# Performance work log

Measured on AMD Instinct MI355X. Metric: run time of the kernel, lower is better.

Reference implementation:

```python
import jax, jax.numpy as jnp
import numpy as np

N = 100_000      # nodes
E = 1_600_000    # edges (before self-loops)
F_IN = 128       # num_features
H = 128          # nhid
G = 512          # graphs in batch
C = 10           # num_classes
EPS = 1e-5       # BatchNorm eps


def setup_inputs() -> dict:
    key = jax.random.key(0)
    ks = jax.random.split(key, 24)
    x = jax.random.normal(ks[0], (N, F_IN), jnp.float32)
    edge_index = jax.random.randint(ks[1], (2, E), 0, N, dtype=jnp.int64)
    batch = jnp.sort(jax.random.randint(ks[2], (N,), 0, G, dtype=jnp.int64))

    def lin(k, fi, fo):
        return jax.random.normal(k, (fi, fo), jnp.float32) / np.sqrt(fi).astype(np.float32)

    inp = dict(x=x, edge_index=edge_index, batch=batch)
    inp.update(
        W1=lin(ks[3], F_IN, H), b1=jnp.zeros((H,), jnp.float32),
        g1=jnp.ones((H,), jnp.float32), be1=jnp.zeros((H,), jnp.float32),
        W2=lin(ks[4], H, H), b2=jnp.zeros((H,), jnp.float32),
        g2=jnp.ones((H,), jnp.float32), be2=jnp.zeros((H,), jnp.float32),
        W3=lin(ks[5], H, H), b3=jnp.zeros((H,), jnp.float32),
        g3=jnp.ones((H,), jnp.float32), be3=jnp.zeros((H,), jnp.float32),
        gp=jnp.ones((H,), jnp.float32), bep=jnp.zeros((H,), jnp.float32),
        lw1=lin(ks[6], H, H), lb1=jnp.zeros((H,), jnp.float32),
        lw2=lin(ks[7], H, C), lb2=jnp.zeros((C,), jnp.float32),
    )
    return inp


def _batchnorm(h, g, b):
    # training-mode BatchNorm1d: batch stats, biased variance
    m = h.mean(axis=0)
    v = h.var(axis=0)
    return g * (h - m) * jax.lax.rsqrt(v + EPS) + b


def _gcn(h, W, b, src, dst, norm, n):
    # GCNConv: h @ W, then normalized gather-scatter aggregation
    h = h @ W
    msg = h[src] * norm[:, None]                     # [E+N, H] gather
    out = jax.ops.segment_sum(msg, dst, num_segments=n)
    return out + b


def reference(x, edge_index, batch, W1, b1, g1, be1, W2, b2, g2, be2,
              W3, b3, g3, be3, gp, bep, lw1, lb1, lw2, lb2):
    n = x.shape[0]
    loops = jnp.arange(n, dtype=edge_index.dtype)
    src = jnp.concatenate([edge_index[0], loops])
    dst = jnp.concatenate([edge_index[1], loops])
    # symmetric normalization D^{-1/2} (A+I) D^{-1/2}
    deg = jax.ops.segment_sum(jnp.ones_like(src, dtype=x.dtype), dst, num_segments=n)
    dis = jnp.where(deg > 0, jax.lax.rsqrt(jnp.maximum(deg, 1.0)), 0.0)
    norm = dis[src] * dis[dst]

    h = jax.nn.relu(_batchnorm(_gcn(x, W1, b1, src, dst, norm, n), g1, be1))
    h = jax.nn.relu(_batchnorm(_gcn(h, W2, b2, src, dst, norm, n), g2, be2))
    h = jax.nn.relu(_batchnorm(_gcn(h, W3, b3, src, dst, norm, n), g3, be3))

    # global_mean_pool over graph ids
    counts = jax.ops.segment_sum(jnp.ones((n,), x.dtype), batch, num_segments=G)
    pooled = jax.ops.segment_sum(h, batch, num_segments=G) / jnp.maximum(counts, 1.0)[:, None]

    z = _batchnorm(pooled, gp, bep)
    z = jax.nn.relu(z @ lw1 + lb1)
    # dropout_ratio=0.0 -> identity
    z = z @ lw2 + lb2
    return jax.nn.log_softmax(z, axis=-1)
```

## Files before the change

kernel.cpp:

```cpp
#include <hip/hip_runtime.h>
#include <hip/hip_bf16.h>
#include <cstdint>

#define HDIM 128

typedef __bf16 bf16x8 __attribute__((ext_vector_type(8)));
typedef unsigned short usx8 __attribute__((ext_vector_type(8)));
typedef float fx4 __attribute__((ext_vector_type(4)));

__device__ __forceinline__ float bf2f(unsigned short u) {
    unsigned int x = ((unsigned int)u) << 16;
    return __uint_as_float(x);
}
__device__ __forceinline__ unsigned short f2bf(float f) {
    unsigned int x = __float_as_uint(f);
    x += 0x7fffu + ((x >> 16) & 1u);
    return (unsigned short)(x >> 16);
}

__device__ __forceinline__ void detect_local(const unsigned int* xw, const unsigned int* eiw,
                                             int& f0, int& f1) {
    int sane = 0;
    for (int k = 0; k < 64; k++) {
        unsigned int w = xw[k];
        unsigned short ss[2] = {(unsigned short)(w & 0xffffu), (unsigned short)(w >> 16)};
        for (int q = 0; q < 2; q++) {
            int e = (ss[q] >> 7) & 0xFF;
            if ((ss[q] & 0x7fffu) == 0 || (e >= 100 && e <= 140)) sane++;
        }
    }
    f0 = (sane >= 110) ? 1 : 0;
    int zeros = 0;
    for (int k = 1; k < 64; k += 2)
        if (eiw[k] == 0) zeros++;
    f1 = (zeros >= 24) ? 1 : 0;
}

struct ParamTab {
    const void* p[15];
    int n[15];
    int off[15];
};

__global__ void phase1(const unsigned int* __restrict__ xw, const unsigned int* __restrict__ eiw,
                       const void* __restrict__ ei, const void* __restrict__ batch,
                       const void* __restrict__ W1, const void* __restrict__ W2,
                       const void* __restrict__ W3, ParamTab tab, int* __restrict__ flags,
                       float* __restrict__ gsumAll, int* __restrict__ Ct,
                       unsigned short* __restrict__ wconv, unsigned short* __restrict__ Wf,
                       int* __restrict__ goff, int* __restrict__ gcnt, int E, int N, int G,
                       int NB, int ntiles, int TILE) {
    __shared__ int h[1024];
    __shared__ int lf0s, lf1s;
    int b = blockIdx.x, t = threadIdx.x;
    if (t == 0) {
        int a0, a1;
        detect_local(xw, eiw, a0, a1);
        lf0s = a0;
        lf1s = a1;
    }
    __syncthreads();
    int lf0 = lf0s, lf1 = lf1s;
    if (b < ntiles) {
        for (int i = t; i < NB; i += 256) h[i] = 0;
        __syncthreads();
        int base = b * TILE;
        for (int i = t; i < TILE; i += 256) {
            int idx = base + i;
            if (idx < E) {
                int d = lf1 ? (int)((const long long*)ei)[(size_t)E + idx]
                            : ((const int*)ei)[(size_t)E + idx];
                atomicAdd(&h[d >> 9], 1);
            }
        }
        __syncthreads();
        for (int k = t; k < NB; k += 256) Ct[k * ntiles + b] = h[k];
    } else if (b < ntiles + 15) {
        int pb = b - ntiles;
        const void* src = tab.p[pb];
        int n = tab.n[pb];
        unsigned short* o = wconv + tab.off[pb];
        if (lf0) {
            const unsigned short* s = (const unsigned short*)src;
            for (int i = t; i < n; i += 256) o[i] = s[i];
        } else {
            const float* s = (const float*)src;
            for (int i = t; i < n; i += 256) o[i] = f2bf(s[i]);
        }
    } else if (b < ntiles + 17) {
        int gi = (b - ntiles - 15) * 256 + t;
        if (gi < G) {
            auto getb = [&](int i) -> int {
                return lf1 ? (int)((const long long*)batch)[i] : ((const int*)batch)[i];
            };
            auto lower = [&](int val) -> int {
                int lo = 0, hi = N;
                while (lo < hi) {
                    int mid = (lo + hi) >> 1;
                    if (getb(mid) < val) lo = mid + 1;
                    else hi = mid;
                }
                return lo;
            };
            int lo = lower(gi), hi = lower(gi + 1);
            goff[gi] = lo;
            gcnt[gi] = hi - lo;
        }
    } else if (b < ntiles + 17 + 24) {
        int idx = (b - ntiles - 17) * 256 + t;
        int layer = idx >> 11;
        int rem = idx & 2047;
        int kt = rem >> 9;
        int nt = (rem >> 6) & 7;
        int lane = rem & 63;
        const void* W = (layer == 0) ? W1 : ((layer == 1) ? W2 : W3);
        int row = lane & 15, quad = lane >> 4;
        unsigned short* o = Wf + ((size_t)layer * 2048 + (size_t)((kt * 8 + nt) * 64 + lane)) * 8;
#pragma unroll
        for (int j = 0; j < 8; j++) {
            int k = kt * 32 + quad * 8 + j;
            int off = k * HDIM + nt * 16 + row;
            o[j] = lf0 ? ((const unsigned short*)W)[off] : f2bf(((const float*)W)[off]);
        }
    } else {
        for (int i = t; i < 6144; i += 256) gsumAll[i] = 0.f;
        if (t == 0) {
            flags[0] = lf0;
            flags[1] = lf1;
        }
    }
}

__global__ void s1_scan(int* __restrict__ Ct, int* __restrict__ btot, int NB, int ntiles) {
    __shared__ int buf[512];
    int b = blockIdx.x, t = threadIdx.x;
    int v = (t < ntiles) ? Ct[b * ntiles + t] : 0;
    buf[t] = v;
    __syncthreads();
    for (int o = 1; o < 512; o <<= 1) {
        int a = (t >= o) ? buf[t - o] : 0;
        __syncthreads();
        buf[t] += a;
        __syncthreads();
    }
    if (t < ntiles) Ct[b * ntiles + t] = buf[t] - v;
    if (t == 0) btot[b] = buf[511];
}

__global__ void p1_scatter(const void* __restrict__ ei, const int* __restrict__ flags,
                           const int* __restrict__ Ct, const int* __restrict__ btot,
                           unsigned int* __restrict__ pairs, int E, int NB, int ntiles,
                           int TILE) {
    __shared__ int cur[1024];
    __shared__ int bb[256];
    int tile = blockIdx.x, t = threadIdx.x;
    int v = (t < NB) ? btot[t] : 0;
    bb[t] = v;
    __syncthreads();
    for (int o = 1; o < 256; o <<= 1) {
        int a = (t >= o) ? bb[t - o] : 0;
        __syncthreads();
        bb[t] += a;
        __syncthreads();
    }
    if (t < NB) cur[t] = (bb[t] - v) + Ct[t * ntiles + tile];
    __syncthreads();
    int base = tile * TILE;
    bool i64 = flags[1] != 0;
    for (int i = t; i < TILE; i += 256) {
        int idx = base + i;
        if (idx < E) {
            int s, d;
            if (i64) {
                s = (int)((const long long*)ei)[idx];
                d = (int)((const long long*)ei)[(size_t)E + idx];
            } else {
                s = ((const int*)ei)[idx];
                d = ((const int*)ei)[(size_t)E + idx];
            }
            int pos = atomicAdd(&cur[d >> 9], 1);
            pairs[pos] = ((unsigned)(d & 511) << 23) | (unsigned)s;
        }
    }
}

__global__ void p2_build(const unsigned int* __restrict__ pairs, const int* __restrict__ btot,
                         int* __restrict__ csrc, int* __restrict__ offs, int* __restrict__ cnt,
                         float* __restrict__ dis, int E, int N, int NB) {
    __shared__ int hist[512];
    __shared__ int start[512];
    __shared__ int cur[512];
    __shared__ int ps[256];
    __shared__ int bb[256];
    __shared__ int sh_excl[256];
    int b = blockIdx.x, t = threadIdx.x;
    int node0 = b * 512;
    int v = (t < NB) ? btot[t] : 0;
    bb[t] = v;
    __syncthreads();
    for (int o = 1; o < 256; o <<= 1) {
        int a = (t >= o) ? bb[t - o] : 0;
        __syncthreads();
        bb[t] += a;
        __syncthreads();
    }
    sh_excl[t] = bb[t] - v;
    for (int i = t; i < 512; i += 256) hist[i] = 0;
    __syncthreads();
    int lo = sh_excl[b];
    int hi = lo + ((b < NB) ? btot[b] : 0);
    for (int i = lo + t; i < hi; i += 256) {
        atomicAdd(&hist[pairs[i] >> 23], 1);
    }
    __syncthreads();
    ps[t] = hist[2 * t] + hist[2 * t + 1];
    __syncthreads();
    for (int o = 1; o < 256; o <<= 1) {
        int a = (t >= o) ? ps[t - o] : 0;
        __syncthreads();
        ps[t] += a;
        __syncthreads();
    }
    int e = t ? ps[t - 1] : 0;
    start[2 * t] = e;
    start[2 * t + 1] = e + hist[2 * t];
    __syncthreads();
    for (int i = t; i < 512; i += 256) {
        cur[i] = 0;
        int node = node0 + i;
        if (node < N) {
            offs[node] = lo + start[i];
            cnt[node] = hist[i];
            dis[node] = rsqrtf((float)(hist[i] + 1));
        }
    }
    __syncthreads();
    for (int i = lo + t; i < hi; i += 256) {
        unsigned int p = pairs[i];
        int l = p >> 23;
        int pos = lo + start[l] + atomicAdd(&cur[l], 1);
        csrc[pos] = (int)(p & 0x7fffffu);
    }
}

__global__ __launch_bounds__(256) void mm_mfma(const void* __restrict__ A,
                                               const unsigned short* __restrict__ Wf,
                                               unsigned short* __restrict__ C, int M,
                                               const float* __restrict__ gsumPrev,
                                               const unsigned short* __restrict__ gamma,
                                               const unsigned short* __restrict__ beta,
                                               const float* __restrict__ dis,
                                               const int* __restrict__ flags, int l0mode,
                                               float invn) {
    __shared__ float scs[128], shs[128];
    __shared__ unsigned short ldsC[4 * 16 * 136];
    int t = threadIdx.x;
    if (!l0mode && t < 128) {
        float s = 0.f, s2 = 0.f;
#pragma unroll
        for (int r = 0; r < 8; r++) {
            s += gsumPrev[r * 256 + t];
            s2 += gsumPrev[r * 256 + 128 + t];
        }
        float m = s * invn;
        float vv = s2 * invn - m * m;
        float sc = bf2f(gamma[t]) * rsqrtf(vv + 1e-5f);
        scs[t] = sc;
        shs[t] = bf2f(beta[t]) - m * sc;
    }
    __syncthreads();
    int gid = blockIdx.x * blockDim.x + t;
    int wave = gid >> 6;
    int lane = t & 63;
    int wv = t >> 6;
    int m0 = wave * 16;
    if (m0 >= M) return;
    int row = lane & 15, quad = lane >> 4;
    bool xfp32 = l0mode && !flags[0];
    const unsigned short* arow = (const unsigned short*)A + (size_t)(m0 + row) * HDIM + quad * 8;
    const float* arowf = (const float*)A + (size_t)(m0 + row) * HDIM + quad * 8;
    fx4 acc[8];
#pragma unroll
    for (int k = 0; k < 8; k++) acc[k] = (fx4){0.f, 0.f, 0.f, 0.f};
#pragma unroll
    for (int kt = 0; kt < 4; kt++) {
        bf16x8 a;
        if (xfp32) {
            fx4 f0 = *(const fx4*)(arowf + kt * 32);
            fx4 f1 = *(const fx4*)(arowf + kt * 32 + 4);
            usx8 tt;
#pragma unroll
            for (int q = 0; q < 4; q++) tt[q] = f2bf(f0[q]);
#pragma unroll
            for (int q = 0; q < 4; q++) tt[4 + q] = f2bf(f1[q]);
            a = __builtin_bit_cast(bf16x8, tt);
        } else {
            usx8 raw = *(const usx8*)(arow + kt * 32);
            if (!l0mode) {
                int col = kt * 32 + quad * 8;
                fx4 s0 = *(const fx4*)&scs[col];
                fx4 s1 = *(const fx4*)&scs[col + 4];
                fx4 h0 = *(const fx4*)&shs[col];
                fx4 h1 = *(const fx4*)&shs[col + 4];
                usx8 tt;
#pragma unroll
                for (int q = 0; q < 4; q++)
                    tt[q] = f2bf(fmaxf(s0[q] * bf2f(raw[q]) + h0[q], 0.f));
#pragma unroll
                for (int q = 0; q < 4; q++)
                    tt[4 + q] = f2bf(fmaxf(s1[q] * bf2f(raw[4 + q]) + h1[q], 0.f));
                a = __builtin_bit_cast(bf16x8, tt);
            } else {
                a = __builtin_bit_cast(bf16x8, raw);
            }
        }
        const unsigned short* wf = Wf + ((size_t)(kt * 8) * 64 + lane) * 8;
#pragma unroll
        for (int nt = 0; nt < 8; nt++) {
            bf16x8 bfr = __builtin_bit_cast(bf16x8, *(const usx8*)(wf + (size_t)nt * 64 * 8));
            acc[nt] = __builtin_amdgcn_mfma_f32_16x16x32_bf16(a, bfr, acc[nt], 0, 0, 0);
        }
    }
    float dsc[4];
#pragma unroll
    for (int r = 0; r < 4; r++) dsc[r] = dis[m0 + quad * 4 + r];
    unsigned short* lw = ldsC + wv * 16 * 136;
#pragma unroll
    for (int nt = 0; nt < 8; nt++) {
        int col = nt * 16 + row;
#pragma unroll
        for (int r = 0; r < 4; r++) {
            lw[(quad * 4 + r) * 136 + col] = f2bf(acc[nt][r] * dsc[r]);
        }
    }
    int row16 = lane >> 2;
    int seg = lane & 3;
    const unsigned short* src = lw + row16 * 136 + seg * 32;
    unsigned short* dst = C + (size_t)(m0 + row16) * HDIM + seg * 32;
#pragma unroll
    for (int k = 0; k < 4; k++) {
        *(usx8*)(dst + k * 8) = *(const usx8*)(src + k * 8);
    }
}

__global__ __launch_bounds__(256) void aggregate(const unsigned short* __restrict__ hw,
                                                 const float* __restrict__ dis,
                                                 const int* __restrict__ offs,
                                                 const int* __restrict__ cnt,
                                                 const int* __restrict__ csrc,
                                                 const unsigned short* __restrict__ bias,
                                                 unsigned short* __restrict__ agg,
                                                 float* __restrict__ gsum8, int n) {
    __shared__ float red[16 * 128];
    int t = threadIdx.x;
    int lane = t & 63;
    int wv = t >> 6;
    int grp = lane >> 4, sub = lane & 15;
    int colb = sub * 8;
    usx8 bv = *(const usx8*)(bias + colb);
    float csum[8], csq[8];
#pragma unroll
    for (int q = 0; q < 8; q++) {
        csum[q] = 0.f;
        csq[q] = 0.f;
    }
    int stride = gridDim.x * 16;
    for (int node = blockIdx.x * 16 + wv * 4 + grp; node < n; node += stride) {
        usx8 sv = *(const usx8*)(hw + (size_t)node * HDIM + colb);
        float a[8];
#pragma unroll
        for (int q = 0; q < 8; q++) a[q] = bf2f(sv[q]);
        int o = offs[node], c = cnt[node];
        int s0 = (c > 0) ? csrc[o] : 0;
        int s1 = (c > 1) ? csrc[o + 1] : 0;
        int s2 = (c > 2) ? csrc[o + 2] : 0;
        int s3 = (c > 3) ? csrc[o + 3] : 0;
        int j = 0;
        while (j < c) {
            usx8 v0 = *(const usx8*)(hw + (size_t)s0 * HDIM + colb);
            usx8 v1 = *(const usx8*)(hw + (size_t)s1 * HDIM + colb);
            usx8 v2 = *(const usx8*)(hw + (size_t)s2 * HDIM + colb);
            usx8 v3 = *(const usx8*)(hw + (size_t)s3 * HDIM + colb);
            s0 = (j + 4 < c) ? csrc[o + j + 4] : 0;
            s1 = (j + 5 < c) ? csrc[o + j + 5] : 0;
            s2 = (j + 6 < c) ? csrc[o + j + 6] : 0;
            s3 = (j + 7 < c) ? csrc[o + j + 7] : 0;
#pragma unroll
            for (int q = 0; q < 8; q++) a[q] += bf2f(v0[q]);
            if (j + 1 < c) {
#pragma unroll
                for (int q = 0; q < 8; q++) a[q] += bf2f(v1[q]);
            }
            if (j + 2 < c) {
#pragma unroll
                for (int q = 0; q < 8; q++) a[q] += bf2f(v2[q]);
            }
            if (j + 3 < c) {
#pragma unroll
                for (int q = 0; q < 8; q++) a[q] += bf2f(v3[q]);
            }
            j += 4;
        }
        float di = dis[node];
        usx8 ov;
#pragma unroll
        for (int q = 0; q < 8; q++) {
            float val = bf2f(bv[q]) + di * a[q];
            ov[q] = f2bf(val);
            float vr = bf2f(ov[q]);
            csum[q] += vr;
            csq[q] += vr * vr;
        }
        *(usx8*)(agg + (size_t)node * HDIM + colb) = ov;
    }
    int gidx = wv * 4 + grp;
    int rep = (blockIdx.x & 7) * 256;
#pragma unroll
    for (int q = 0; q < 8; q++) red[gidx * 128 + colb + q] = csum[q];
    __syncthreads();
    if (t < 128) {
        float s = 0.f;
#pragma unroll
        for (int g = 0; g < 16; g++) s += red[g * 128 + t];
        atomicAdd(&gsum8[rep + t], s);
    }
    __syncthreads();
#pragma unroll
    for (int q = 0; q < 8; q++) red[gidx * 128 + colb + q] = csq[q];
    __syncthreads();
    if (t < 128) {
        float s = 0.f;
#pragma unroll
        for (int g = 0; g < 16; g++) s += red[g * 128 + t];
        atomicAdd(&gsum8[rep + 128 + t], s);
    }
}

__global__ void pool(const unsigned short* __restrict__ hin, const int* __restrict__ goff,
                     const int* __restrict__ gcnt, const float* __restrict__ gsum3,
                     const unsigned short* __restrict__ gamma,
                     const unsigned short* __restrict__ beta, float* __restrict__ pooled,
                     float invn) {
    __shared__ float scs[128], shs[128];
    __shared__ float ls[256];
    int g = blockIdx.x, t = threadIdx.x;
    if (t < 128) {
        float s = 0.f, s2 = 0.f;
#pragma unroll
        for (int r = 0; r < 8; r++) {
            s += gsum3[r * 256 + t];
            s2 += gsum3[r * 256 + 128 + t];
        }
        float m = s * invn;
        float vv = s2 * invn - m * m;
        float sc = bf2f(gamma[t]) * rsqrtf(vv + 1e-5f);
        scs[t] = sc;
        shs[t] = bf2f(beta[t]) - m * sc;
    }
    __syncthreads();
    int c = t & 127, p = t >> 7;
    float scale = scs[c], shift = shs[c];
    int s = goff[g], cn = gcnt[g];
    float acc = 0.f;
    for (int r = s + p; r < s + cn; r += 2)
        acc += fmaxf(scale * bf2f(hin[(size_t)r * HDIM + c]) + shift, 0.f);
    ls[t] = acc;
    __syncthreads();
    if (t < 128) pooled[(size_t)g * HDIM + t] = (ls[t] + ls[t + 128]) / fmaxf((float)cn, 1.f);
}
__global__ void pooled_bn(const float* __restrict__ pooled, const unsigned short* __restrict__ g,
                          const unsigned short* __restrict__ be, float* __restrict__ psc,
                          float* __restrict__ psh, int G_) {
    int t = threadIdx.x;
    int c = t & 127, p = t >> 7;
    float s = 0.f, s2 = 0.f;
    for (int r = p; r < G_; r += 4) {
        float v = pooled[(size_t)r * HDIM + c];
        s += v;
        s2 += v * v;
    }
    __shared__ float ls[512], ls2[512];
    ls[t] = s;
    ls2[t] = s2;
    __syncthreads();
    if (t < 128) {
        float S = ls[t] + ls[t + 128] + ls[t + 256] + ls[t + 384];
        float S2 = ls2[t] + ls2[t + 128] + ls2[t + 256] + ls2[t + 384];
        float m = S / (float)G_;
        float v = S2 / (float)G_ - m * m;
        float sc = bf2f(g[t]) * rsqrtf(v + 1e-5f);
        psc[t] = sc;
        psh[t] = bf2f(be[t]) - m * sc;
    }
}
__global__ void mlp12(const float* __restrict__ pooled, const float* __restrict__ psc,
                      const float* __restrict__ psh, const unsigned short* __restrict__ lw1,
                      const unsigned short* __restrict__ lb1,
                      const unsigned short* __restrict__ lw2,
                      const unsigned short* __restrict__ lb2, void* __restrict__ out,
                      const int* __restrict__ flags) {
    int r = blockIdx.x, t = threadIdx.x;
    __shared__ float row[128];
    __shared__ float z1s[128];
    __shared__ float z2[10];
    __shared__ float lse;
    row[t] = psc[t] * pooled[(size_t)r * HDIM + t] + psh[t];
    __syncthreads();
    float acc = bf2f(lb1[t]);
    for (int k = 0; k < 128; k++) acc += row[k] * bf2f(lw1[k * HDIM + t]);
    z1s[t] = fmaxf(acc, 0.f);
    __syncthreads();
    if (t < 10) {
        float a = bf2f(lb2[t]);
        for (int k = 0; k < 128; k++) a += z1s[k] * bf2f(lw2[k * 10 + t]);
        z2[t] = a;
    }
    __syncthreads();
    if (t == 0) {
        float m = z2[0];
        for (int j = 1; j < 10; j++) m = fmaxf(m, z2[j]);
        float s = 0.f;
        for (int j = 0; j < 10; j++) s += expf(z2[j] - m);
        lse = m + logf(s);
    }
    __syncthreads();
    if (t < 10) {
        float v = z2[t] - lse;
        if (flags[0]) ((unsigned short*)out)[r * 10 + t] = f2bf(v);
        else ((float*)out)[r * 10 + t] = v;
    }
}

extern "C" void kernel_launch(void* const* d_in, const int* in_sizes, int n_in,
                              void* d_out, int out_size, void* d_ws, size_t ws_size,
                              hipStream_t stream) {
    const void* x = d_in[0];
    const void* ei = d_in[1];
    const void* batch = d_in[2];

    int N_ = in_sizes[2];
    int E_ = in_sizes[1] / 2;
    int G_ = out_size / 10;

    const int TILE = 4096;
    int NB = (N_ + 511) / 512;
    int ntiles = (E_ + TILE - 1) / TILE;
    int L = NB * ntiles;

    char* ws = (char*)d_ws;
    auto alloc = [&](size_t bytes) -> char* {
        char* p = ws;
        ws += (bytes + 255) & ~(size_t)255;
        return p;
    };
    int* flags = (int*)alloc(256);
    float* dis = (float*)alloc((size_t)N_ * 4);
    int* offs = (int*)alloc((size_t)N_ * 4);
    int* cnt = (int*)alloc((size_t)N_ * 4);
    int* Ct = (int*)alloc((size_t)L * 4);
    int* btot = (int*)alloc(1024);
    unsigned int* pairs = (unsigned int*)alloc((size_t)E_ * 4);
    int* csrc = (int*)alloc((size_t)E_ * 4);
    unsigned short* hw = (unsigned short*)alloc((size_t)N_ * HDIM * 2);
    unsigned short* aggbuf = (unsigned short*)alloc((size_t)N_ * HDIM * 2);
    unsigned short* wconv = (unsigned short*)alloc(70000 * 2);
    unsigned short* wfrag = (unsigned short*)alloc(3 * HDIM * HDIM * 2);
    float* gsumAll = (float*)alloc(6144 * 4);
    int* gcnt = (int*)alloc((size_t)G_ * 4);
    int* goff = (int*)alloc((size_t)G_ * 4);
    float* pooled = (float*)alloc((size_t)G_ * HDIM * 4);
    float* psc = (float*)alloc(128 * 4);
    float* psh = (float*)alloc(128 * 4);

    const int oB = 49152;
    const int oLB1 = oB + 1408;
    const int oLW1 = oLB1 + 128;
    const int oLW2 = oLW1 + 16384;
    const int oLB2 = oLW2 + 1280;

    ParamTab tab;
    const int srcIdx[15] = {4, 5, 6, 8, 9, 10, 12, 13, 14, 15, 16, 18, 17, 19, 20};
    const int dstOff[15] = {oB + 0, oB + 128, oB + 256,
                            oB + 384, oB + 512, oB + 640,
                            oB + 768, oB + 896, oB + 1024,
                            oB + 1152, oB + 1280,
                            oLB1, oLW1, oLW2, oLB2};
    for (int i = 0; i < 15; i++) {
        tab.p[i] = d_in[srcIdx[i]];
        tab.n[i] = in_sizes[srcIdx[i]];
        tab.off[i] = dstOff[i];
    }

    int p1_grid = ntiles + 15 + 2 + 24 + 1;
    phase1<<<p1_grid, 256, 0, stream>>>((const unsigned int*)x, (const unsigned int*)ei, ei,
                                        batch, d_in[3], d_in[7], d_in[11], tab, flags, gsumAll,
                                        Ct, wconv, wfrag, goff, gcnt, E_, N_, G_, NB, ntiles,
                                        TILE);
    s1_scan<<<NB, 512, 0, stream>>>(Ct, btot, NB, ntiles);
    p1_scatter<<<ntiles, 256, 0, stream>>>(ei, flags, Ct, btot, pairs, E_, NB, ntiles, TILE);
    p2_build<<<NB, 256, 0, stream>>>(pairs, btot, csrc, offs, cnt, dis, E_, N_, NB);

    int mm_blocks = (((N_ + 15) / 16) * 64 + 255) / 256;
    float invn = 1.f / (float)N_;

    for (int l = 0; l < 3; l++) {
        const void* A = (l == 0) ? x : (const void*)aggbuf;
        const float* gp = (l == 0) ? nullptr : (gsumAll + (size_t)(l - 1) * 2048);
        const unsigned short* gam = wconv + oB + (l ? (l - 1) * 384 + 128 : 0);
        const unsigned short* bet = wconv + oB + (l ? (l - 1) * 384 + 256 : 0);
        mm_mfma<<<mm_blocks, 256, 0, stream>>>(A, wfrag + (size_t)l * HDIM * HDIM, hw, N_, gp,
                                               gam, bet, dis, flags, (l == 0) ? 1 : 0, invn);
        aggregate<<<768, 256, 0, stream>>>(hw, dis, offs, cnt, csrc, wconv + oB + l * 384,
                                           aggbuf, gsumAll + (size_t)l * 2048, N_);
    }

    pool<<<G_, 256, 0, stream>>>(aggbuf, goff, gcnt, gsumAll + 2 * 2048,
                                 wconv + oB + 2 * 384 + 128, wconv + oB + 2 * 384 + 256, pooled,
                                 invn);
    pooled_bn<<<1, 512, 0, stream>>>(pooled, wconv + oB + 1152, wconv + oB + 1280, psc, psh, G_);
    mlp12<<<G_, 128, 0, stream>>>(pooled, psc, psh, wconv + oLW1, wconv + oLB1, wconv + oLW2,
                                  wconv + oLB2, d_out, flags);
}
```

Baseline: 514.5 us.

## Fuse all stages into one persistent megakernel with grid-wide barriers

Replaces the sequence of around fourteen kernel launches (CSR build, three matmul and aggregate layers, pooling, BN and MLP) with a single persistent kernel of 512 blocks. The stages are separated by a custom hierarchical atomic grid barrier. This is meant to remove launch overhead and inter-kernel gaps. In exchange, the matmul and aggregate phases run on a fixed grid with grid-stride loops, and correctness depends on all 512 blocks being co-resident (launch_bounds of 2 blocks per CU). The barrier-reset handshake through a magic word could also race across repeated calls.

```diff
diff --git a/kernel.cpp b/kernel.cpp
--- a/kernel.cpp
+++ b/kernel.cpp
@@ -3,6 +3,8 @@
 #include <cstdint>
 
 #define HDIM 128
+#define GRID 512
+#define MAGIC 0x13572468u
 
 typedef __bf16 bf16x8 __attribute__((ext_vector_type(8)));
 typedef unsigned short usx8 __attribute__((ext_vector_type(8)));
@@ -36,50 +38,115 @@
     f1 = (zeros >= 24) ? 1 : 0;
 }
 
+__device__ __forceinline__ void gbar(unsigned int* bar, int id) {
+    __syncthreads();
+    if (threadIdx.x == 0) {
+        unsigned int* B = bar + id * 256;
+        int j = blockIdx.x & 7;
+        unsigned int old =
+            __hip_atomic_fetch_add(&B[j * 16], 1u, __ATOMIC_ACQ_REL, __HIP_MEMORY_SCOPE_AGENT);
+        bool released = false;
+        if (old == (GRID / 8 - 1)) {
+            unsigned int m =
+                __hip_atomic_fetch_add(&B[128], 1u, __ATOMIC_ACQ_REL, __HIP_MEMORY_SCOPE_AGENT);
+            if (m == 7u) {
+                __hip_atomic_store(&B[144], 1u, __ATOMIC_RELEASE, __HIP_MEMORY_SCOPE_AGENT);
+                released = true;
+            }
+        }
+        if (!released) {
+            while (__hip_atomic_load(&B[144], __ATOMIC_ACQUIRE, __HIP_MEMORY_SCOPE_AGENT) == 0u) {
+                __builtin_amdgcn_s_sleep(16);
+            }
+        }
+    }
+    __syncthreads();
+}
+
 struct ParamTab {
     const void* p[15];
     int n[15];
     int off[15];
 };
 
-__global__ void phase1(const unsigned int* __restrict__ xw, const unsigned int* __restrict__ eiw,
-                       const void* __restrict__ ei, const void* __restrict__ batch,
-                       const void* __restrict__ W1, const void* __restrict__ W2,
-                       const void* __restrict__ W3, ParamTab tab, int* __restrict__ flags,
-                       float* __restrict__ gsumAll, int* __restrict__ Ct,
-                       unsigned short* __restrict__ wconv, unsigned short* __restrict__ Wf,
-                       int* __restrict__ goff, int* __restrict__ gcnt, int E, int N, int G,
-                       int NB, int ntiles, int TILE) {
-    __shared__ int h[1024];
-    __shared__ int lf0s, lf1s;
-    int b = blockIdx.x, t = threadIdx.x;
+struct MegaParams {
+    const void* x;
+    const void* ei;
+    const void* batch;
+    const void* W1;
+    const void* W2;
+    const void* W3;
+    ParamTab tab;
+    unsigned int* bar;
+    float* gsumAll;
+    int* Ct;
+    int* btot;
+    int* goff;
+    int* gcnt;
+    int* csrc;
+    int* offs;
+    int* cnt;
+    float* dis;
+    unsigned int* pairs;
+    unsigned short* wconv;
+    unsigned short* wfrag;
+    unsigned short* hw;
+    unsigned short* aggbuf;
+    float* pooled;
+    float* psc;
+    float* psh;
+    void* out;
+    int E, N, G, NB, ntiles, TILE;
+    float invn;
+};
+
+#define oB 49152
+
+__global__ __launch_bounds__(256, 2) void mega(MegaParams P) {
+    __shared__ __align__(16) unsigned char smem[18688];
+    __shared__ int lfs[2];
+    const int b = blockIdx.x, t = threadIdx.x;
+    unsigned int* bar = P.bar;
+
+    if (b == 0) {
+        for (int i = t; i < 4096; i += 256)
+            __hip_atomic_store(&bar[i], 0u, __ATOMIC_RELAXED, __HIP_MEMORY_SCOPE_AGENT);
+        __syncthreads();
+        if (t == 0)
+            __hip_atomic_store(&bar[4096], MAGIC, __ATOMIC_RELEASE, __HIP_MEMORY_SCOPE_AGENT);
+    }
     if (t == 0) {
         int a0, a1;
-        detect_local(xw, eiw, a0, a1);
-        lf0s = a0;
-        lf1s = a1;
+        detect_local((const unsigned int*)P.x, (const unsigned int*)P.ei, a0, a1);
+        lfs[0] = a0;
+        lfs[1] = a1;
+        while (__hip_atomic_load(&bar[4096], __ATOMIC_ACQUIRE, __HIP_MEMORY_SCOPE_AGENT) != MAGIC) {
+            __builtin_amdgcn_s_sleep(16);
+        }
     }
     __syncthreads();
-    int lf0 = lf0s, lf1 = lf1s;
-    if (b < ntiles) {
-        for (int i = t; i < NB; i += 256) h[i] = 0;
-        __syncthreads();
-        int base = b * TILE;
-        for (int i = t; i < TILE; i += 256) {
+    const int lf0 = lfs[0], lf1 = lfs[1];
+    const int* ei32 = (const int*)P.ei;
+
+    if (b < P.ntiles) {
+        int* h = (int*)smem;
+        for (int i = t; i < P.NB; i += 256) h[i] = 0;
+        __syncthreads();
+        int base = b * P.TILE;
+        for (int i = t; i < P.TILE; i += 256) {
             int idx = base + i;
-            if (idx < E) {
-                int d = lf1 ? (int)((const long long*)ei)[(size_t)E + idx]
-                            : ((const int*)ei)[(size_t)E + idx];
+            if (idx < P.E) {
+                int d = lf1 ? ei32[2 * ((size_t)P.E + idx)] : ei32[(size_t)P.E + idx];
                 atomicAdd(&h[d >> 9], 1);
             }
         }
         __syncthreads();
-        for (int k = t; k < NB; k += 256) Ct[k * ntiles + b] = h[k];
-    } else if (b < ntiles + 15) {
-        int pb = b - ntiles;
-        const void* src = tab.p[pb];
-        int n = tab.n[pb];
-        unsigned short* o = wconv + tab.off[pb];
+        for (int k = t; k < P.NB; k += 256) P.Ct[k * P.ntiles + b] = h[k];
+    } else if (b < P.ntiles + 15) {
+        int pb = b - P.ntiles;
+        const void* src = P.tab.p[pb];
+        int n = P.tab.n[pb];
+        unsigned short* o = P.wconv + P.tab.off[pb];
         if (lf0) {
             const unsigned short* s = (const unsigned short*)src;
             for (int i = t; i < n; i += 256) o[i] = s[i];
@@ -87,14 +154,14 @@
             const float* s = (const float*)src;
             for (int i = t; i < n; i += 256) o[i] = f2bf(s[i]);
         }
-    } else if (b < ntiles + 17) {
-        int gi = (b - ntiles - 15) * 256 + t;
-        if (gi < G) {
+    } else if (b < P.ntiles + 17) {
+        int gi = (b - P.ntiles - 15) * 256 + t;
+        if (gi < P.G) {
             auto getb = [&](int i) -> int {
-                return lf1 ? (int)((const long long*)batch)[i] : ((const int*)batch)[i];
+                return lf1 ? (int)((const long long*)P.batch)[i] : ((const int*)P.batch)[i];
             };
             auto lower = [&](int val) -> int {
-                int lo = 0, hi = N;
+                int lo = 0, hi = P.N;
                 while (lo < hi) {
                     int mid = (lo + hi) >> 1;
                     if (getb(mid) < val) lo = mid + 1;
@@ -103,446 +170,442 @@
                 return lo;
             };
             int lo = lower(gi), hi = lower(gi + 1);
-            goff[gi] = lo;
-            gcnt[gi] = hi - lo;
-        }
-    } else if (b < ntiles + 17 + 24) {
-        int idx = (b - ntiles - 17) * 256 + t;
+            P.goff[gi] = lo;
+            P.gcnt[gi] = hi - lo;
+        }
+    } else if (b < P.ntiles + 41) {
+        int idx = (b - P.ntiles - 17) * 256 + t;
         int layer = idx >> 11;
         int rem = idx & 2047;
-        int kt = rem >> 9;
-        int nt = (rem >> 6) & 7;
-        int lane = rem & 63;
-        const void* W = (layer == 0) ? W1 : ((layer == 1) ? W2 : W3);
+        int kt = rem >> 9, nt = (rem >> 6) & 7, lane = rem & 63;
+        const void* W = (layer == 0) ? P.W1 : ((layer == 1) ? P.W2 : P.W3);
         int row = lane & 15, quad = lane >> 4;
-        unsigned short* o = Wf + ((size_t)layer * 2048 + (size_t)((kt * 8 + nt) * 64 + lane)) * 8;
+        unsigned short* o =
+            P.wfrag + ((size_t)layer * 2048 + (size_t)((kt * 8 + nt) * 64 + lane)) * 8;
 #pragma unroll
         for (int j = 0; j < 8; j++) {
             int k = kt * 32 + quad * 8 + j;
             int off = k * HDIM + nt * 16 + row;
             o[j] = lf0 ? ((const unsigned short*)W)[off] : f2bf(((const float*)W)[off]);
         }
-    } else {
-        for (int i = t; i < 6144; i += 256) gsumAll[i] = 0.f;
-        if (t == 0) {
-            flags[0] = lf0;
-            flags[1] = lf1;
-        }
-    }
-}
-
-__global__ void s1_scan(int* __restrict__ Ct, int* __restrict__ btot, int NB, int ntiles) {
-    __shared__ int buf[512];
-    int b = blockIdx.x, t = threadIdx.x;
-    int v = (t < ntiles) ? Ct[b * ntiles + t] : 0;
-    buf[t] = v;
-    __syncthreads();
-    for (int o = 1; o < 512; o <<= 1) {
-        int a = (t >= o) ? buf[t - o] : 0;
-        __syncthreads();
-        buf[t] += a;
-        __syncthreads();
-    }
-    if (t < ntiles) Ct[b * ntiles + t] = buf[t] - v;
-    if (t == 0) btot[b] = buf[511];
-}
-
-__global__ void p1_scatter(const void* __restrict__ ei, const int* __restrict__ flags,
-                           const int* __restrict__ Ct, const int* __restrict__ btot,
-                           unsigned int* __restrict__ pairs, int E, int NB, int ntiles,
-                           int TILE) {
-    __shared__ int cur[1024];
-    __shared__ int bb[256];
-    int tile = blockIdx.x, t = threadIdx.x;
-    int v = (t < NB) ? btot[t] : 0;
-    bb[t] = v;
-    __syncthreads();
-    for (int o = 1; o < 256; o <<= 1) {
-        int a = (t >= o) ? bb[t - o] : 0;
-        __syncthreads();
-        bb[t] += a;
-        __syncthreads();
-    }
-    if (t < NB) cur[t] = (bb[t] - v) + Ct[t * ntiles + tile];
-    __syncthreads();
-    int base = tile * TILE;
-    bool i64 = flags[1] != 0;
-    for (int i = t; i < TILE; i += 256) {
-        int idx = base + i;
-        if (idx < E) {
-            int s, d;
-            if (i64) {
-                s = (int)((const long long*)ei)[idx];
-                d = (int)((const long long*)ei)[(size_t)E + idx];
-            } else {
-                s = ((const int*)ei)[idx];
-                d = ((const int*)ei)[(size_t)E + idx];
-            }
-            int pos = atomicAdd(&cur[d >> 9], 1);
-            pairs[pos] = ((unsigned)(d & 511) << 23) | (unsigned)s;
-        }
-    }
-}
-
-__global__ void p2_build(const unsigned int* __restrict__ pairs, const int* __restrict__ btot,
-                         int* __restrict__ csrc, int* __restrict__ offs, int* __restrict__ cnt,
-                         float* __restrict__ dis, int E, int N, int NB) {
-    __shared__ int hist[512];
-    __shared__ int start[512];
-    __shared__ int cur[512];
-    __shared__ int ps[256];
-    __shared__ int bb[256];
-    __shared__ int sh_excl[256];
-    int b = blockIdx.x, t = threadIdx.x;
-    int node0 = b * 512;
-    int v = (t < NB) ? btot[t] : 0;
-    bb[t] = v;
-    __syncthreads();
-    for (int o = 1; o < 256; o <<= 1) {
-        int a = (t >= o) ? bb[t - o] : 0;
-        __syncthreads();
-        bb[t] += a;
-        __syncthreads();
-    }
-    sh_excl[t] = bb[t] - v;
-    for (int i = t; i < 512; i += 256) hist[i] = 0;
-    __syncthreads();
-    int lo = sh_excl[b];
-    int hi = lo + ((b < NB) ? btot[b] : 0);
-    for (int i = lo + t; i < hi; i += 256) {
-        atomicAdd(&hist[pairs[i] >> 23], 1);
-    }
-    __syncthreads();
-    ps[t] = hist[2 * t] + hist[2 * t + 1];
-    __syncthreads();
-    for (int o = 1; o < 256; o <<= 1) {
-        int a = (t >= o) ? ps[t - o] : 0;
-        __syncthreads();
-        ps[t] += a;
-        __syncthreads();
-    }
-    int e = t ? ps[t - 1] : 0;
-    start[2 * t] = e;
-    start[2 * t + 1] = e + hist[2 * t];
-    __syncthreads();
-    for (int i = t; i < 512; i += 256) {
-        cur[i] = 0;
-        int node = node0 + i;
-        if (node < N) {
-            offs[node] = lo + start[i];
-            cnt[node] = hist[i];
-            dis[node] = rsqrtf((float)(hist[i] + 1));
-        }
-    }
-    __syncthreads();
-    for (int i = lo + t; i < hi; i += 256) {
-        unsigned int p = pairs[i];
-        int l = p >> 23;
-        int pos = lo + start[l] + atomicAdd(&cur[l], 1);
-        csrc[pos] = (int)(p & 0x7fffffu);
-    }
-}
-
-__global__ __launch_bounds__(256) void mm_mfma(const void* __restrict__ A,
-                                               const unsigned short* __restrict__ Wf,
-                                               unsigned short* __restrict__ C, int M,
-                                               const float* __restrict__ gsumPrev,
-                                               const unsigned short* __restrict__ gamma,
-                                               const unsigned short* __restrict__ beta,
-                                               const float* __restrict__ dis,
-                                               const int* __restrict__ flags, int l0mode,
-                                               float invn) {
-    __shared__ float scs[128], shs[128];
-    __shared__ unsigned short ldsC[4 * 16 * 136];
-    int t = threadIdx.x;
-    if (!l0mode && t < 128) {
+    } else if (b == P.ntiles + 41) {
+        for (int i = t; i < 6144; i += 256) P.gsumAll[i] = 0.f;
+    }
+    gbar(bar, 0);
+
+    if (b < P.NB) {
+        int* buf = (int*)smem;
+        int base = b * P.ntiles;
+        int v0 = (2 * t < P.ntiles) ? P.Ct[base + 2 * t] : 0;
+        int v1 = (2 * t + 1 < P.ntiles) ? P.Ct[base + 2 * t + 1] : 0;
+        int s = v0 + v1;
+        buf[t] = s;
+        __syncthreads();
+        for (int o = 1; o < 256; o <<= 1) {
+            int a = (t >= o) ? buf[t - o] : 0;
+            __syncthreads();
+            buf[t] += a;
+            __syncthreads();
+        }
+        int excl = buf[t] - s;
+        if (2 * t < P.ntiles) P.Ct[base + 2 * t] = excl;
+        if (2 * t + 1 < P.ntiles) P.Ct[base + 2 * t + 1] = excl + v0;
+        if (t == 255) P.btot[b] = buf[255];
+    }
+    gbar(bar, 1);
+
+    if (b < P.ntiles) {
+        int* cur = (int*)smem;
+        int* bb = (int*)(smem + 4096);
+        int v = (t < P.NB) ? P.btot[t] : 0;
+        bb[t] = v;
+        __syncthreads();
+        for (int o = 1; o < 256; o <<= 1) {
+            int a = (t >= o) ? bb[t - o] : 0;
+            __syncthreads();
+            bb[t] += a;
+            __syncthreads();
+        }
+        if (t < P.NB) cur[t] = (bb[t] - v) + P.Ct[t * P.ntiles + b];
+        __syncthreads();
+        int base = b * P.TILE;
+        for (int i = t; i < P.TILE; i += 256) {
+            int idx = base + i;
+            if (idx < P.E) {
+                int s, d;
+                if (lf1) {
+                    s = ei32[2 * (size_t)idx];
+                    d = ei32[2 * ((size_t)P.E + idx)];
+                } else {
+                    s = ei32[idx];
+                    d = ei32[(size_t)P.E + idx];
+                }
+                int pos = atomicAdd(&cur[d >> 9], 1);
+                P.pairs[pos] = ((unsigned)(d & 511) << 23) | (unsigned)s;
+            }
+        }
+    }
+    gbar(bar, 2);
+
+    if (b < P.NB) {
+        int* hist = (int*)smem;
+        int* start = (int*)(smem + 2048);
+        int* cur = (int*)(smem + 4096);
+        int* ps = (int*)(smem + 6144);
+        int* bb = (int*)(smem + 7168);
+        int node0 = b * 512;
+        int v = (t < P.NB) ? P.btot[t] : 0;
+        bb[t] = v;
+        __syncthreads();
+        for (int o = 1; o < 256; o <<= 1) {
+            int a = (t >= o) ? bb[t - o] : 0;
+            __syncthreads();
+            bb[t] += a;
+            __syncthreads();
+        }
+        int lo = bb[b] - P.btot[b];
+        int hi = lo + P.btot[b];
+        for (int i = t; i < 512; i += 256) hist[i] = 0;
+        __syncthreads();
+        for (int i = lo + t; i < hi; i += 256) atomicAdd(&hist[P.pairs[i] >> 23], 1);
+        __syncthreads();
+        ps[t] = hist[2 * t] + hist[2 * t + 1];
+        __syncthreads();
+        for (int o = 1; o < 256; o <<= 1) {
+            int a = (t >= o) ? ps[t - o] : 0;
+            __syncthreads();
+            ps[t] += a;
+            __syncthreads();
+        }
+        int e = t ? ps[t - 1] : 0;
+        start[2 * t] = e;
+        start[2 * t + 1] = e + hist[2 * t];
+        __syncthreads();
+        for (int i = t; i < 512; i += 256) {
+            cur[i] = 0;
+            int node = node0 + i;
+            if (node < P.N) {
+                P.offs[node] = lo + start[i];
+                P.cnt[node] = hist[i];
+                P.dis[node] = rsqrtf((float)(hist[i] + 1));
+            }
+        }
+        __syncthreads();
+        for (int i = lo + t; i < hi; i += 256) {
+            unsigned int p = P.pairs[i];
+            int l = p >> 23;
+            int pos = lo + start[l] + atomicAdd(&cur[l], 1);
+            P.csrc[pos] = (int)(p & 0x7fffffu);
+        }
+    }
+    gbar(bar, 3);
+
+    for (int l = 0; l < 3; l++) {
+        {
+            float* scs = (float*)smem;
+            float* shs = (float*)(smem + 512);
+            unsigned short* ldsC = (unsigned short*)(smem + 1024);
+            if (l && t < 128) {
+                const float* gp = P.gsumAll + (size_t)(l - 1) * 2048;
+                float s = 0.f, s2 = 0.f;
+#pragma unroll
+                for (int r = 0; r < 8; r++) {
+                    s += gp[r * 256 + t];
+                    s2 += gp[r * 256 + 128 + t];
+                }
+                const unsigned short* gam = P.wconv + oB + (l - 1) * 384 + 128;
+                const unsigned short* bet = P.wconv + oB + (l - 1) * 384 + 256;
+                float m = s * P.invn;
+                float vv = s2 * P.invn - m * m;
+                float sc = bf2f(gam[t]) * rsqrtf(vv + 1e-5f);
+                scs[t] = sc;
+                shs[t] = bf2f(bet[t]) - m * sc;
+            }
+            __syncthreads();
+            const unsigned short* Wf = P.wfrag + (size_t)l * HDIM * HDIM;
+            int lane = t & 63, wv = t >> 6;
+            int row = lane & 15, quad = lane >> 4;
+            bool xfp32 = (l == 0) && !lf0;
+            const unsigned short* Abase = (l == 0) ? (const unsigned short*)P.x : P.aggbuf;
+            int nmt = (P.N + 15) >> 4;
+            for (int tile = b * 4 + wv; tile < nmt; tile += GRID * 4) {
+                int m0 = tile * 16;
+                const unsigned short* arow = Abase + (size_t)(m0 + row) * HDIM + quad * 8;
+                const float* arowf = (const float*)P.x + (size_t)(m0 + row) * HDIM + quad * 8;
+                fx4 acc[8];
+#pragma unroll
+                for (int k = 0; k < 8; k++) acc[k] = (fx4){0.f, 0.f, 0.f, 0.f};
+#pragma unroll
+                for (int kt = 0; kt < 4; kt++) {
+                    bf16x8 a;
+                    if (xfp32) {
+                        fx4 f0 = *(const fx4*)(arowf + kt * 32);
+                        fx4 f1 = *(const fx4*)(arowf + kt * 32 + 4);
+                        usx8 tt;
+#pragma unroll
+                        for (int q = 0; q < 4; q++) tt[q] = f2bf(f0[q]);
+#pragma unroll
+                        for (int q = 0; q < 4; q++) tt[4 + q] = f2bf(f1[q]);
+                        a = __builtin_bit_cast(bf16x8, tt);
+                    } else {
+                        usx8 raw = *(const usx8*)(arow + kt * 32);
+                        if (l) {
+                            int col = kt * 32 + quad * 8;
+                            fx4 s0 = *(const fx4*)&scs[col];
+                            fx4 s1 = *(const fx4*)&scs[col + 4];
+                            fx4 h0 = *(const fx4*)&shs[col];
+                            fx4 h1 = *(const fx4*)&shs[col + 4];
+                            usx8 tt;
+#pragma unroll
+                            for (int q = 0; q < 4; q++)
+                                tt[q] = f2bf(fmaxf(s0[q] * bf2f(raw[q]) + h0[q], 0.f));
+#pragma unroll
+                            for (int q = 0; q < 4; q++)
+                                tt[4 + q] = f2bf(fmaxf(s1[q] * bf2f(raw[4 + q]) + h1[q], 0.f));
+                            a = __builtin_bit_cast(bf16x8, tt);
+                        } else {
+                            a = __builtin_bit_cast(bf16x8, raw);
+                        }
+                    }
+                    const unsigned short* wf = Wf + ((size_t)(kt * 8) * 64 + lane) * 8;
+#pragma unroll
+                    for (int nt = 0; nt < 8; nt++) {
+                        bf16x8 bfr =
+                            __builtin_bit_cast(bf16x8, *(const usx8*)(wf + (size_t)nt * 64 * 8));
+                        acc[nt] =
+                            __builtin_amdgcn_mfma_f32_16x16x32_bf16(a, bfr, acc[nt], 0, 0, 0);
+                    }
+                }
+                float dsc[4];
+#pragma unroll
+                for (int r = 0; r < 4; r++) dsc[r] = P.dis[m0 + quad * 4 + r];
+                unsigned short* lw = ldsC + wv * 16 * 136;
+#pragma unroll
+                for (int nt = 0; nt < 8; nt++) {
+                    int col = nt * 16 + row;
+#pragma unroll
+                    for (int r = 0; r < 4; r++) {
+                        lw[(quad * 4 + r) * 136 + col] = f2bf(acc[nt][r] * dsc[r]);
+                    }
+                }
+                int row16 = lane >> 2;
+                int seg = lane & 3;
+                const unsigned short* src = lw + row16 * 136 + seg * 32;
+                unsigned short* dst = P.hw + (size_t)(m0 + row16) * HDIM + seg * 32;
+#pragma unroll
+                for (int k = 0; k < 4; k++) {
+                    *(usx8*)(dst + k * 8) = *(const usx8*)(src + k * 8);
+                }
+            }
+        }
+        gbar(bar, 4 + 2 * l);
+
+        {
+            float* red = (float*)smem;
+            int lane = t & 63, wv = t >> 6;
+            int grp = lane >> 4, sub = lane & 15;
+            int colb = sub * 8;
+            const unsigned short* bias = P.wconv + oB + l * 384;
+            usx8 bv = *(const usx8*)(bias + colb);
+            float csum[8], csq[8];
+#pragma unroll
+            for (int q = 0; q < 8; q++) {
+                csum[q] = 0.f;
+                csq[q] = 0.f;
+            }
+            int stride = GRID * 16;
+            for (int node = b * 16 + wv * 4 + grp; node < P.N; node += stride) {
+                usx8 sv = *(const usx8*)(P.hw + (size_t)node * HDIM + colb);
+                float a[8];
+#pragma unroll
+                for (int q = 0; q < 8; q++) a[q] = bf2f(sv[q]);
+                int o = P.offs[node], c = P.cnt[node];
+                int s0 = (c > 0) ? P.csrc[o] : 0;
+                int s1 = (c > 1) ? P.csrc[o + 1] : 0;
+                int s2 = (c > 2) ? P.csrc[o + 2] : 0;
+                int s3 = (c > 3) ? P.csrc[o + 3] : 0;
+                int j = 0;
+                while (j < c) {
+                    usx8 v0 = *(const usx8*)(P.hw + (size_t)s0 * HDIM + colb);
+                    usx8 v1 = *(const usx8*)(P.hw + (size_t)s1 * HDIM + colb);
+                    usx8 v2 = *(const usx8*)(P.hw + (size_t)s2 * HDIM + colb);
+                    usx8 v3 = *(const usx8*)(P.hw + (size_t)s3 * HDIM + colb);
+                    s0 = (j + 4 < c) ? P.csrc[o + j + 4] : 0;
+                    s1 = (j + 5 < c) ? P.csrc[o + j + 5] : 0;
+                    s2 = (j + 6 < c) ? P.csrc[o + j + 6] : 0;
+                    s3 = (j + 7 < c) ? P.csrc[o + j + 7] : 0;
+#pragma unroll
+                    for (int q = 0; q < 8; q++) a[q] += bf2f(v0[q]);
+                    if (j + 1 < c) {
+#pragma unroll
+                        for (int q = 0; q < 8; q++) a[q] += bf2f(v1[q]);
+                    }
+                    if (j + 2 < c) {
+#pragma unroll
+                        for (int q = 0; q < 8; q++) a[q] += bf2f(v2[q]);
+                    }
+                    if (j + 3 < c) {
+#pragma unroll
+                        for (int q = 0; q < 8; q++) a[q] += bf2f(v3[q]);
+                    }
+                    j += 4;
+                }
+                float di = P.dis[node];
+                usx8 ov;
+#pragma unroll
+                for (int q = 0; q < 8; q++) {
+                    float val = bf2f(bv[q]) + di * a[q];
+                    ov[q] = f2bf(val);
+                    float vr = bf2f(ov[q]);
+                    csum[q] += vr;
+                    csq[q] += vr * vr;
+                }
+                *(usx8*)(P.aggbuf + (size_t)node * HDIM + colb) = ov;
+            }
+            float* gsum8 = P.gsumAll + (size_t)l * 2048;
+            int gidx = wv * 4 + grp;
+            int rep = (b & 7) * 256;
+            __syncthreads();
+#pragma unroll
+            for (int q = 0; q < 8; q++) red[gidx * 128 + colb + q] = csum[q];
+            __syncthreads();
+            if (t < 128) {
+                float s = 0.f;
+#pragma unroll
+                for (int g = 0; g < 16; g++) s += red[g * 128 + t];
+                atomicAdd(&gsum8[rep + t], s);
+            }
+            __syncthreads();
+#pragma unroll
+            for (int q = 0; q < 8; q++) red[gidx * 128 + colb + q] = csq[q];
+            __syncthreads();
+            if (t < 128) {
+                float s = 0.f;
+#pragma unroll
+                for (int g = 0; g < 16; g++) s += red[g * 128 + t];
+                atomicAdd(&gsum8[rep + 128 + t], s);
+            }
+        }
+        gbar(bar, 5 + 2 * l);
+    }
+
+    {
+        float* scs = (float*)smem;
+        float* shs = (float*)(smem + 512);
+        float* ls = (float*)(smem + 1024);
+        if (t < 128) {
+            const float* gp = P.gsumAll + 2 * 2048;
+            float s = 0.f, s2 = 0.f;
+#pragma unroll
+            for (int r = 0; r < 8; r++) {
+                s += gp[r * 256 + t];
+                s2 += gp[r * 256 + 128 + t];
+            }
+            const unsigned short* gam = P.wconv + oB + 2 * 384 + 128;
+            const unsigned short* bet = P.wconv + oB + 2 * 384 + 256;
+            float m = s * P.invn;
+            float vv = s2 * P.invn - m * m;
+            float sc = bf2f(gam[t]) * rsqrtf(vv + 1e-5f);
+            scs[t] = sc;
+            shs[t] = bf2f(bet[t]) - m * sc;
+        }
+        __syncthreads();
+        for (int g = b; g < P.G; g += GRID) {
+            int c = t & 127, pp = t >> 7;
+            float scale = scs[c], shift = shs[c];
+            int s = P.goff[g], cn = P.gcnt[g];
+            float acc = 0.f;
+            for (int r = s + pp; r < s + cn; r += 2)
+                acc += fmaxf(scale * bf2f(P.aggbuf[(size_t)r * HDIM + c]) + shift, 0.f);
+            ls[t] = acc;
+            __syncthreads();
+            if (t < 128)
+                P.pooled[(size_t)g * HDIM + t] = (ls[t] + ls[t + 128]) / fmaxf((float)cn, 1.f);
+            __syncthreads();
+        }
+    }
+    gbar(bar, 10);
+
+    if (b == 0) {
+        float* ls = (float*)smem;
+        float* ls2 = (float*)(smem + 1024);
+        int c = t & 127, pp = t >> 7;
         float s = 0.f, s2 = 0.f;
-#pragma unroll
-        for (int r = 0; r < 8; r++) {
-            s += gsumPrev[r * 256 + t];
-            s2 += gsumPrev[r * 256 + 128 + t];
-        }
-        float m = s * invn;
-        float vv = s2 * invn - m * m;
-        float sc = bf2f(gamma[t]) * rsqrtf(vv + 1e-5f);
-        scs[t] = sc;
-        shs[t] = bf2f(beta[t]) - m * sc;
-    }
-    __syncthreads();
-    int gid = blockIdx.x * blockDim.x + t;
-    int wave = gid >> 6;
-    int lane = t & 63;
-    int wv = t >> 6;
-    int m0 = wave * 16;
-    if (m0 >= M) return;
-    int row = lane & 15, quad = lane >> 4;
-    bool xfp32 = l0mode && !flags[0];
-    const unsigned short* arow = (const unsigned short*)A + (size_t)(m0 + row) * HDIM + quad * 8;
-    const float* arowf = (const float*)A + (size_t)(m0 + row) * HDIM + quad * 8;
-    fx4 acc[8];
-#pragma unroll
-    for (int k = 0; k < 8; k++) acc[k] = (fx4){0.f, 0.f, 0.f, 0.f};
-#pragma unroll
-    for (int kt = 0; kt < 4; kt++) {
-        bf16x8 a;
-        if (xfp32) {
-            fx4 f0 = *(const fx4*)(arowf + kt * 32);
-            fx4 f1 = *(const fx4*)(arowf + kt * 32 + 4);
-            usx8 tt;
-#pragma unroll
-            for (int q = 0; q < 4; q++) tt[q] = f2bf(f0[q]);
-#pragma unroll
-            for (int q = 0; q < 4; q++) tt[4 + q] = f2bf(f1[q]);
-            a = __builtin_bit_cast(bf16x8, tt);
-        } else {
-            usx8 raw = *(const usx8*)(arow + kt * 32);
-            if (!l0mode) {
-                int col = kt * 32 + quad * 8;
-                fx4 s0 = *(const fx4*)&scs[col];
-                fx4 s1 = *(const fx4*)&scs[col + 4];
-                fx4 h0 = *(const fx4*)&shs[col];
-                fx4 h1 = *(const fx4*)&shs[col + 4];
-                usx8 tt;
-#pragma unroll
-                for (int q = 0; q < 4; q++)
-                    tt[q] = f2bf(fmaxf(s0[q] * bf2f(raw[q]) + h0[q], 0.f));
-#pragma unroll
-                for (int q = 0; q < 4; q++)
-                    tt[4 + q] = f2bf(fmaxf(s1[q] * bf2f(raw[4 + q]) + h1[q], 0.f));
-                a = __builtin_bit_cast(bf16x8, tt);
-            } else {
-                a = __builtin_bit_cast(bf16x8, raw);
-            }
-        }
-        const unsigned short* wf = Wf + ((size_t)(kt * 8) * 64 + lane) * 8;
-#pragma unroll
-        for (int nt = 0; nt < 8; nt++) {
-            bf16x8 bfr = __builtin_bit_cast(bf16x8, *(const usx8*)(wf + (size_t)nt * 64 * 8));
-            acc[nt] = __builtin_amdgcn_mfma_f32_16x16x32_bf16(a, bfr, acc[nt], 0, 0, 0);
-        }
-    }
-    float dsc[4];
-#pragma unroll
-    for (int r = 0; r < 4; r++) dsc[r] = dis[m0 + quad * 4 + r];
-    unsigned short* lw = ldsC + wv * 16 * 136;
-#pragma unroll
-    for (int nt = 0; nt < 8; nt++) {
-        int col = nt * 16 + row;
-#pragma unroll
-        for (int r = 0; r < 4; r++) {
-            lw[(quad * 4 + r) * 136 + col] = f2bf(acc[nt][r] * dsc[r]);
-        }
-    }
-    int row16 = lane >> 2;
-    int seg = lane & 3;
-    const unsigned short* src = lw + row16 * 136 + seg * 32;
-    unsigned short* dst = C + (size_t)(m0 + row16) * HDIM + seg * 32;
-#pragma unroll
-    for (int k = 0; k < 4; k++) {
-        *(usx8*)(dst + k * 8) = *(const usx8*)(src + k * 8);
-    }
-}
-
-__global__ __launch_bounds__(256) void aggregate(const unsigned short* __restrict__ hw,
-                                                 const float* __restrict__ dis,
-                                                 const int* __restrict__ offs,
-                                                 const int* __restrict__ cnt,
-                                                 const int* __restrict__ csrc,
-                                                 const unsigned short* __restrict__ bias,
-                                                 unsigned short* __restrict__ agg,
-                                                 float* __restrict__ gsum8, int n) {
-    __shared__ float red[16 * 128];
-    int t = threadIdx.x;
-    int lane = t & 63;
-    int wv = t >> 6;
-    int grp = lane >> 4, sub = lane & 15;
-    int colb = sub * 8;
-    usx8 bv = *(const usx8*)(bias + colb);
-    float csum[8], csq[8];
-#pragma unroll
-    for (int q = 0; q < 8; q++) {
-        csum[q] = 0.f;
-        csq[q] = 0.f;
-    }
-    int stride = gridDim.x * 16;
-    for (int node = blockIdx.x * 16 + wv * 4 + grp; node < n; node += stride) {
-        usx8 sv = *(const usx8*)(hw + (size_t)node * HDIM + colb);
-        float a[8];
-#pragma unroll
-        for (int q = 0; q < 8; q++) a[q] = bf2f(sv[q]);
-        int o = offs[node], c = cnt[node];
-        int s0 = (c > 0) ? csrc[o] : 0;
-        int s1 = (c > 1) ? csrc[o + 1] : 0;
-        int s2 = (c > 2) ? csrc[o + 2] : 0;
-        int s3 = (c > 3) ? csrc[o + 3] : 0;
-        int j = 0;
-        while (j < c) {
-            usx8 v0 = *(const usx8*)(hw + (size_t)s0 * HDIM + colb);
-            usx8 v1 = *(const usx8*)(hw + (size_t)s1 * HDIM + colb);
-            usx8 v2 = *(const usx8*)(hw + (size_t)s2 * HDIM + colb);
-            usx8 v3 = *(const usx8*)(hw + (size_t)s3 * HDIM + colb);
-            s0 = (j + 4 < c) ? csrc[o + j + 4] : 0;
-            s1 = (j + 5 < c) ? csrc[o + j + 5] : 0;
-            s2 = (j + 6 < c) ? csrc[o + j + 6] : 0;
-            s3 = (j + 7 < c) ? csrc[o + j + 7] : 0;
-#pragma unroll
-            for (int q = 0; q < 8; q++) a[q] += bf2f(v0[q]);
-            if (j + 1 < c) {
-#pragma unroll
-                for (int q = 0; q < 8; q++) a[q] += bf2f(v1[q]);
-            }
-            if (j + 2 < c) {
-#pragma unroll
-                for (int q = 0; q < 8; q++) a[q] += bf2f(v2[q]);
-            }
-            if (j + 3 < c) {
-#pragma unroll
-                for (int q = 0; q < 8; q++) a[q] += bf2f(v3[q]);
-            }
-            j += 4;
-        }
-        float di = dis[node];
-        usx8 ov;
-#pragma unroll
-        for (int q = 0; q < 8; q++) {
-            float val = bf2f(bv[q]) + di * a[q];
-            ov[q] = f2bf(val);
-            float vr = bf2f(ov[q]);
-            csum[q] += vr;
-            csq[q] += vr * vr;
-        }
-        *(usx8*)(agg + (size_t)node * HDIM + colb) = ov;
-    }
-    int gidx = wv * 4 + grp;
-    int rep = (blockIdx.x & 7) * 256;
-#pragma unroll
-    for (int q = 0; q < 8; q++) red[gidx * 128 + colb + q] = csum[q];
-    __syncthreads();
-    if (t < 128) {
-        float s = 0.f;
-#pragma unroll
-        for (int g = 0; g < 16; g++) s += red[g * 128 + t];
-        atomicAdd(&gsum8[rep + t], s);
-    }
-    __syncthreads();
-#pragma unroll
-    for (int q = 0; q < 8; q++) red[gidx * 128 + colb + q] = csq[q];
-    __syncthreads();
-    if (t < 128) {
-        float s = 0.f;
-#pragma unroll
-        for (int g = 0; g < 16; g++) s += red[g * 128 + t];
-        atomicAdd(&gsum8[rep + 128 + t], s);
-    }
-}
-
-__global__ void pool(const unsigned short* __restrict__ hin, const int* __restrict__ goff,
-                     const int* __restrict__ gcnt, const float* __restrict__ gsum3,
-                     const unsigned short* __restrict__ gamma,
-                     const unsigned short* __restrict__ beta, float* __restrict__ pooled,
-                     float invn) {
-    __shared__ float scs[128], shs[128];
-    __shared__ float ls[256];
-    int g = blockIdx.x, t = threadIdx.x;
-    if (t < 128) {
-        float s = 0.f, s2 = 0.f;
-#pragma unroll
-        for (int r = 0; r < 8; r++) {
-            s += gsum3[r * 256 + t];
-            s2 += gsum3[r * 256 + 128 + t];
-        }
-        float m = s * invn;
-        float vv = s2 * invn - m * m;
-        float sc = bf2f(gamma[t]) * rsqrtf(vv + 1e-5f);
-        scs[t] = sc;
-        shs[t] = bf2f(beta[t]) - m * sc;
-    }
-    __syncthreads();
-    int c = t & 127, p = t >> 7;
-    float scale = scs[c], shift = shs[c];
-    int s = goff[g], cn = gcnt[g];
-    float acc = 0.f;
-    for (int r = s + p; r < s + cn; r += 2)
-        acc += fmaxf(scale * bf2f(hin[(size_t)r * HDIM + c]) + shift, 0.f);
-    ls[t] = acc;
-    __syncthreads();
-    if (t < 128) pooled[(size_t)g * HDIM + t] = (ls[t] + ls[t + 128]) / fmaxf((float)cn, 1.f);
-}
-__global__ void pooled_bn(const float* __restrict__ pooled, const unsigned short* __restrict__ g,
-                          const unsigned short* __restrict__ be, float* __restrict__ psc,
-                          float* __restrict__ psh, int G_) {
-    int t = threadIdx.x;
-    int c = t & 127, p = t >> 7;
-    float s = 0.f, s2 = 0.f;
-    for (int r = p; r < G_; r += 4) {
-        float v = pooled[(size_t)r * HDIM + c];
-        s += v;
-        s2 += v * v;
-    }
-    __shared__ float ls[512], ls2[512];
-    ls[t] = s;
-    ls2[t] = s2;
-    __syncthreads();
-    if (t < 128) {
-        float S = ls[t] + ls[t + 128] + ls[t + 256] + ls[t + 384];
-        float S2 = ls2[t] + ls2[t + 128] + ls2[t + 256] + ls2[t + 384];
-        float m = S / (float)G_;
-        float v = S2 / (float)G_ - m * m;
-        float sc = bf2f(g[t]) * rsqrtf(v + 1e-5f);
-        psc[t] = sc;
-        psh[t] = bf2f(be[t]) - m * sc;
-    }
-}
-__global__ void mlp12(const float* __restrict__ pooled, const float* __restrict__ psc,
-                      const float* __restrict__ psh, const unsigned short* __restrict__ lw1,
-                      const unsigned short* __restrict__ lb1,
-                      const unsigned short* __restrict__ lw2,
-                      const unsigned short* __restrict__ lb2, void* __restrict__ out,
-                      const int* __restrict__ flags) {
-    int r = blockIdx.x, t = threadIdx.x;
-    __shared__ float row[128];
-    __shared__ float z1s[128];
-    __shared__ float z2[10];
-    __shared__ float lse;
-    row[t] = psc[t] * pooled[(size_t)r * HDIM + t] + psh[t];
-    __syncthreads();
-    float acc = bf2f(lb1[t]);
-    for (int k = 0; k < 128; k++) acc += row[k] * bf2f(lw1[k * HDIM + t]);
-    z1s[t] = fmaxf(acc, 0.f);
-    __syncthreads();
-    if (t < 10) {
-        float a = bf2f(lb2[t]);
-        for (int k = 0; k < 128; k++) a += z1s[k] * bf2f(lw2[k * 10 + t]);
-        z2[t] = a;
-    }
-    __syncthreads();
-    if (t == 0) {
-        float m = z2[0];
-        for (int j = 1; j < 10; j++) m = fmaxf(m, z2[j]);
-        float s = 0.f;
-        for (int j = 0; j < 10; j++) s += expf(z2[j] - m);
-        lse = m + logf(s);
-    }
-    __syncthreads();
-    if (t < 10) {
-        float v = z2[t] - lse;
-        if (flags[0]) ((unsigned short*)out)[r * 10 + t] = f2bf(v);
-        else ((float*)out)[r * 10 + t] = v;
+        for (int r = pp; r < P.G; r += 2) {
+            float v = P.pooled[(size_t)r * HDIM + c];
+            s += v;
+            s2 += v * v;
+        }
+        ls[t] = s;
+        ls2[t] = s2;
+        __syncthreads();
+        if (t < 128) {
+            float S = ls[t] + ls[t + 128];
+            float S2 = ls2[t] + ls2[t + 128];
+            float m = S / (float)P.G;
+            float v = S2 / (float)P.G - m * m;
+            const unsigned short* gp = P.wconv + oB + 1152;
+            const unsigned short* bep = P.wconv + oB + 1280;
+            float sc = bf2f(gp[t]) * rsqrtf(v + 1e-5f);
+            P.psc[t] = sc;
+            P.psh[t] = bf2f(bep[t]) - m * sc;
+        }
+    }
+    gbar(bar, 11);
+
+    {
+        const int oLB1 = oB + 1408;
+        const int oLW1 = oLB1 + 128;
+        const int oLW2 = oLW1 + 16384;
+        const int oLB2 = oLW2 + 1280;
+        float* row = (float*)smem;
+        float* z1s = (float*)(smem + 512);
+        float* z2 = (float*)(smem + 1024);
+        float* lsep = (float*)(smem + 1088);
+        for (int g = b; g < P.G; g += GRID) {
+            if (t < 128) row[t] = P.psc[t] * P.pooled[(size_t)g * HDIM + t] + P.psh[t];
+            __syncthreads();
+            if (t < 128) {
+                const unsigned short* lw1 = P.wconv + oLW1;
+                float acc = bf2f(P.wconv[oLB1 + t]);
+                for (int k = 0; k < 128; k++) acc += row[k] * bf2f(lw1[k * HDIM + t]);
+                z1s[t] = fmaxf(acc, 0.f);
+            }
+            __syncthreads();
+            if (t < 10) {
+                const unsigned short* lw2 = P.wconv + oLW2;
+                float a = bf2f(P.wconv[oLB2 + t]);
+                for (int k = 0; k < 128; k++) a += z1s[k] * bf2f(lw2[k * 10 + t]);
+                z2[t] = a;
+            }
+            __syncthreads();
+            if (t == 0) {
+                float m = z2[0];
+                for (int j = 1; j < 10; j++) m = fmaxf(m, z2[j]);
+                float s = 0.f;
+                for (int j = 0; j < 10; j++) s += expf(z2[j] - m);
+                *lsep = m + logf(s);
+            }
+            __syncthreads();
+            if (t < 10) {
+                float v = z2[t] - *lsep;
+                if (lf0) ((unsigned short*)P.out)[g * 10 + t] = f2bf(v);
+                else ((float*)P.out)[g * 10 + t] = v;
+            }
+            __syncthreads();
+        }
     }
 }
 
 extern "C" void kernel_launch(void* const* d_in, const int* in_sizes, int n_in,
                               void* d_out, int out_size, void* d_ws, size_t ws_size,
                               hipStream_t stream) {
-    const void* x = d_in[0];
-    const void* ei = d_in[1];
-    const void* batch = d_in[2];
-
     int N_ = in_sizes[2];
     int E_ = in_sizes[1] / 2;
     int G_ = out_size / 10;
 
-    const int TILE = 4096;
+    int TILE = 4096;
+    while ((E_ + TILE - 1) / TILE + 42 > GRID) TILE *= 2;
     int NB = (N_ + 511) / 512;
     int ntiles = (E_ + TILE - 1) / TILE;
     int L = NB * ntiles;
@@ -553,32 +616,44 @@
         ws += (bytes + 255) & ~(size_t)255;
         return p;
     };
-    int* flags = (int*)alloc(256);
-    float* dis = (float*)alloc((size_t)N_ * 4);
-    int* offs = (int*)alloc((size_t)N_ * 4);
-    int* cnt = (int*)alloc((size_t)N_ * 4);
-    int* Ct = (int*)alloc((size_t)L * 4);
-    int* btot = (int*)alloc(1024);
-    unsigned int* pairs = (unsigned int*)alloc((size_t)E_ * 4);
-    int* csrc = (int*)alloc((size_t)E_ * 4);
-    unsigned short* hw = (unsigned short*)alloc((size_t)N_ * HDIM * 2);
-    unsigned short* aggbuf = (unsigned short*)alloc((size_t)N_ * HDIM * 2);
-    unsigned short* wconv = (unsigned short*)alloc(70000 * 2);
-    unsigned short* wfrag = (unsigned short*)alloc(3 * HDIM * HDIM * 2);
-    float* gsumAll = (float*)alloc(6144 * 4);
-    int* gcnt = (int*)alloc((size_t)G_ * 4);
-    int* goff = (int*)alloc((size_t)G_ * 4);
-    float* pooled = (float*)alloc((size_t)G_ * HDIM * 4);
-    float* psc = (float*)alloc(128 * 4);
-    float* psh = (float*)alloc(128 * 4);
-
-    const int oB = 49152;
+    MegaParams P;
+    P.bar = (unsigned int*)alloc(4200 * 4);
+    P.x = d_in[0];
+    P.ei = d_in[1];
+    P.batch = d_in[2];
+    P.W1 = d_in[3];
+    P.W2 = d_in[7];
+    P.W3 = d_in[11];
+    P.dis = (float*)alloc((size_t)N_ * 4);
+    P.offs = (int*)alloc((size_t)N_ * 4);
+    P.cnt = (int*)alloc((size_t)N_ * 4);
+    P.Ct = (int*)alloc((size_t)L * 4);
+    P.btot = (int*)alloc(1024);
+    P.pairs = (unsigned int*)alloc((size_t)E_ * 4);
+    P.csrc = (int*)alloc((size_t)E_ * 4);
+    P.hw = (unsigned short*)alloc((size_t)N_ * HDIM * 2);
+    P.aggbuf = (unsigned short*)alloc((size_t)N_ * HDIM * 2);
+    P.wconv = (unsigned short*)alloc(70000 * 2);
+    P.wfrag = (unsigned short*)alloc(3 * HDIM * HDIM * 2);
+    P.gsumAll = (float*)alloc(6144 * 4);
+    P.gcnt = (int*)alloc((size_t)G_ * 4);
+    P.goff = (int*)alloc((size_t)G_ * 4);
+    P.pooled = (float*)alloc((size_t)G_ * HDIM * 4);
+    P.psc = (float*)alloc(128 * 4);
+    P.psh = (float*)alloc(128 * 4);
+    P.out = d_out;
+    P.E = E_;
+    P.N = N_;
+    P.G = G_;
+    P.NB = NB;
+    P.ntiles = ntiles;
+    P.TILE = TILE;
+    P.invn = 1.f / (float)N_;
+
     const int oLB1 = oB + 1408;
     const int oLW1 = oLB1 + 128;
     const int oLW2 = oLW1 + 16384;
     const int oLB2 = oLW2 + 1280;
-
-    ParamTab tab;
     const int srcIdx[15] = {4, 5, 6, 8, 9, 10, 12, 13, 14, 15, 16, 18, 17, 19, 20};
     const int dstOff[15] = {oB + 0, oB + 128, oB + 256,
                             oB + 384, oB + 512, oB + 640,
@@ -586,38 +661,10 @@
                             oB + 1152, oB + 1280,
                             oLB1, oLW1, oLW2, oLB2};
     for (int i = 0; i < 15; i++) {
-        tab.p[i] = d_in[srcIdx[i]];
-        tab.n[i] = in_sizes[srcIdx[i]];
-        tab.off[i] = dstOff[i];
-    }
-
-    int p1_grid = ntiles + 15 + 2 + 24 + 1;
-    phase1<<<p1_grid, 256, 0, stream>>>((const unsigned int*)x, (const unsigned int*)ei, ei,
-                                        batch, d_in[3], d_in[7], d_in[11], tab, flags, gsumAll,
-                                        Ct, wconv, wfrag, goff, gcnt, E_, N_, G_, NB, ntiles,
-                                        TILE);
-    s1_scan<<<NB, 512, 0, stream>>>(Ct, btot, NB, ntiles);
-    p1_scatter<<<ntiles, 256, 0, stream>>>(ei, flags, Ct, btot, pairs, E_, NB, ntiles, TILE);
-    p2_build<<<NB, 256, 0, stream>>>(pairs, btot, csrc, offs, cnt, dis, E_, N_, NB);
-
-    int mm_blocks = (((N_ + 15) / 16) * 64 + 255) / 256;
-    float invn = 1.f / (float)N_;
-
-    for (int l = 0; l < 3; l++) {
-        const void* A = (l == 0) ? x : (const void*)aggbuf;
-        const float* gp = (l == 0) ? nullptr : (gsumAll + (size_t)(l - 1) * 2048);
-        const unsigned short* gam = wconv + oB + (l ? (l - 1) * 384 + 128 : 0);
-        const unsigned short* bet = wconv + oB + (l ? (l - 1) * 384 + 256 : 0);
-        mm_mfma<<<mm_blocks, 256, 0, stream>>>(A, wfrag + (size_t)l * HDIM * HDIM, hw, N_, gp,
-                                               gam, bet, dis, flags, (l == 0) ? 1 : 0, invn);
-        aggregate<<<768, 256, 0, stream>>>(hw, dis, offs, cnt, csrc, wconv + oB + l * 384,
-                                           aggbuf, gsumAll + (size_t)l * 2048, N_);
-    }
-
-    pool<<<G_, 256, 0, stream>>>(aggbuf, goff, gcnt, gsumAll + 2 * 2048,
-                                 wconv + oB + 2 * 384 + 128, wconv + oB + 2 * 384 + 256, pooled,
-                                 invn);
-    pooled_bn<<<1, 512, 0, stream>>>(pooled, wconv + oB + 1152, wconv + oB + 1280, psc, psh, G_);
-    mlp12<<<G_, 128, 0, stream>>>(pooled, psc, psh, wconv + oLW1, wconv + oLB1, wconv + oLW2,
-                                  wconv + oLB2, d_out, flags);
+        P.tab.p[i] = d_in[srcIdx[i]];
+        P.tab.n[i] = in_sizes[srcIdx[i]];
+        P.tab.off[i] = dstOff[i];
+    }
+
+    mega<<<GRID, 256, 0, stream>>>(P);
 }
```

Measured after the change: 1.707 ms. +231.8%, slower.
